# Optimization experiments

Measured on AMD Instinct MI355X. Metric: run time of the kernel, lower is better.

Reference implementation:

```python
import jax, jax.numpy as jnp
import numpy as np

# FP4 (e2m1) value table: sign bit in code>>3, magnitude in code&7
FP4 = jnp.array([0.0, 0.5, 1.0, 1.5, 2.0, 3.0, 4.0, 6.0,
                 -0.0, -0.5, -1.0, -1.5, -2.0, -3.0, -4.0, -6.0], dtype=jnp.float32)
BLOCK = 32  # MX block size: one shared E8M0 scale per 32 elements


def _unpack(packed):
    # packed: int32 holding byte values 0..255; low nibble first
    lo = packed & 0xF
    hi = (packed >> 4) & 0xF
    return jnp.stack([lo, hi], axis=-1).reshape(*packed.shape[:-1], packed.shape[-1] * 2)


def _dequant(packed, sf):
    # packed: [..., N//2] packed FP4 codes; sf: [..., N//32] E8M0 exponents
    vals = FP4[_unpack(packed)]                       # [..., N]
    n = vals.shape[-1]
    scale = jnp.exp2(sf.astype(jnp.float32) - 127.0)  # [..., N//32]
    vals = vals.reshape(*vals.shape[:-1], n // BLOCK, BLOCK) * scale[..., None]
    return vals.reshape(*scale.shape[:-1], n)


def setup_inputs() -> dict:
    key = jax.random.key(0)
    ks = jax.random.split(key, 6)
    M, IN, OUT, R = 8192, 4096, 4096, 128
    return {
        "x_q": jax.random.randint(ks[0], (M, IN // 2), 0, 256, dtype=jnp.int32),
        "scales_x": jax.random.randint(ks[1], (M, IN // BLOCK), 120, 134, dtype=jnp.int32),
        "weight": jax.random.randint(ks[2], (OUT, IN // 2), 0, 256, dtype=jnp.int32),
        "SF_w": jax.random.randint(ks[3], (OUT * IN // BLOCK,), 120, 134, dtype=jnp.int32),
        "low_rank_weight": jax.random.randint(ks[4], (OUT, R // 2), 0, 256, dtype=jnp.int32),
        "SF_low_rank_weight": jax.random.randint(ks[5], (OUT * R // BLOCK,), 120, 134, dtype=jnp.int32),
    }


def reference(x_q, scales_x, weight, SF_w, low_rank_weight, SF_low_rank_weight):
    OUT = weight.shape[0]
    IN = weight.shape[1] * 2
    R = low_rank_weight.shape[1] * 2  # 128
    # Low-rank path: first R unpacked features of x (R//2 packed bytes, R//32 scale blocks)
    x_lr = _dequant(x_q[:, :R // 2], scales_x[:, :R // BLOCK])                    # [M, R]
    W_lr = _dequant(low_rank_weight, SF_low_rank_weight.reshape(OUT, R // BLOCK))  # [OUT, R]
    out = jnp.einsum('mr,or->mo', x_lr, W_lr, preferred_element_type=jnp.float32)
    # Main 4-bit matmul fused with the low-rank correction
    x = _dequant(x_q, scales_x)                               # [M, IN]
    W = _dequant(weight, SF_w.reshape(OUT, IN // BLOCK))      # [OUT, IN]
    out = out + jnp.einsum('mi,oi->mo', x, W, preferred_element_type=jnp.float32)
    return out
```

## Files before the change

### kernel.cpp

```cpp
#include <hip/hip_runtime.h>
#include <hip/hip_bf16.h>
#include <stdint.h>


#define M_DIM 8192
#define N_DIM 4096
#define K_MAIN 4096
#define K_TOT 4224
#define NCHUNK 132
#define NT 33

#define XP_OFF   ((size_t)0)
#define WP_OFF   (XP_OFF + (size_t)NCHUNK * M_DIM * 16)
#define SXH_OFF  (WP_OFF + (size_t)NCHUNK * N_DIM * 16)
#define SWH_OFF  (SXH_OFF + (size_t)NT * 2 * M_DIM * 2)
#define WS_NEED  (SWH_OFF + (size_t)NT * 2 * N_DIM * 2)

typedef __attribute__((ext_vector_type(4))) float f32x4;
typedef __attribute__((ext_vector_type(16))) float f32x16;
typedef __attribute__((ext_vector_type(8))) short short8;
typedef __attribute__((ext_vector_type(8))) _Float16 half8;
typedef __attribute__((ext_vector_type(4))) int i32x4;
typedef __attribute__((ext_vector_type(8))) int i32x8;

#define PXP_N (NCHUNK * M_DIM)
#define PWP_N (NCHUNK * N_DIM)
#define TSX_N (NT * 2 * M_DIM / 2)
#define TSW_N (NT * 2 * N_DIM / 2)
#define PACK_TOTAL (PXP_N + PWP_N + TSX_N + TSW_N)

__device__ inline unsigned pack4(i32x4 q) {
    return (q.x & 255) | ((q.y & 255) << 8) | ((q.z & 255) << 16) |
           ((unsigned)(q.w & 255) << 24);
}

__global__ __launch_bounds__(256)
void pack_kernel(const int* __restrict__ xq, const int* __restrict__ sx,
                 const int* __restrict__ w, const int* __restrict__ sfw,
                 const int* __restrict__ lrw, const int* __restrict__ sflr,
                 uint8_t* __restrict__ ws) {
    int t = blockIdx.x * 256 + threadIdx.x;
    if (t < PXP_N) {
        const int g = t >> 13;
        const int m = t & 8191;
        const int gs = (g < 128) ? g : (g - 128);
        const int* src = xq + (size_t)m * 2048 + gs * 16;
        i32x4 o;
        o.x = (int)pack4(*(const i32x4*)(src + 0));
        o.y = (int)pack4(*(const i32x4*)(src + 4));
        o.z = (int)pack4(*(const i32x4*)(src + 8));
        o.w = (int)pack4(*(const i32x4*)(src + 12));
        *(i32x4*)(ws + XP_OFF + ((size_t)g * M_DIM + m) * 16) = o;
    } else if (t < PXP_N + PWP_N) {
        const int i = t - PXP_N;
        const int g = i >> 12;
        const int n = i & 4095;
        const int* src = (g < 128) ? (w + (size_t)n * 2048 + g * 16)
                                   : (lrw + (size_t)n * 64 + (g - 128) * 16);
        i32x4 o;
        o.x = (int)pack4(*(const i32x4*)(src + 0));
        o.y = (int)pack4(*(const i32x4*)(src + 4));
        o.z = (int)pack4(*(const i32x4*)(src + 8));
        o.w = (int)pack4(*(const i32x4*)(src + 12));
        *(i32x4*)(ws + WP_OFF + ((size_t)g * N_DIM + n) * 16) = o;
    } else if (t < PXP_N + PWP_N + TSX_N) {
        int i = t - PXP_N - PWP_N;
        int plane = i >> 12;
        int kt = plane >> 1, h = plane & 1;
        int r2 = (i & 4095) << 1;
        int g0 = kt * 4 + h, g2 = g0 + 2;
        int s0 = (g0 < 128) ? g0 : g0 - 128;
        int s2 = (g2 < 128) ? g2 : g2 - 128;
        unsigned b0 = sx[(size_t)r2 * 128 + s0] & 255;
        unsigned b1 = sx[(size_t)r2 * 128 + s2] & 255;
        unsigned b2 = sx[(size_t)(r2 + 1) * 128 + s0] & 255;
        unsigned b3 = sx[(size_t)(r2 + 1) * 128 + s2] & 255;
        *(unsigned*)(ws + SXH_OFF + (size_t)i * 4) = b0 | (b1 << 8) | (b2 << 16) | (b3 << 24);
    } else if (t < PACK_TOTAL) {
        int i = t - PXP_N - PWP_N - TSX_N;
        int plane = i >> 11;
        int kt = plane >> 1, h = plane & 1;
        int r2 = (i & 2047) << 1;
        int g0 = kt * 4 + h, g2 = g0 + 2;
        unsigned b0, b1, b2, b3;
        if (g0 < 128) { b0 = sfw[(size_t)r2 * 128 + g0] & 255; b2 = sfw[(size_t)(r2 + 1) * 128 + g0] & 255; }
        else          { b0 = sflr[(size_t)r2 * 4 + (g0 - 128)] & 255; b2 = sflr[(size_t)(r2 + 1) * 4 + (g0 - 128)] & 255; }
        if (g2 < 128) { b1 = sfw[(size_t)r2 * 128 + g2] & 255; b3 = sfw[(size_t)(r2 + 1) * 128 + g2] & 255; }
        else          { b1 = sflr[(size_t)r2 * 4 + (g2 - 128)] & 255; b3 = sflr[(size_t)(r2 + 1) * 4 + (g2 - 128)] & 255; }
        *(unsigned*)(ws + SWH_OFF + (size_t)i * 4) = b0 | (b1 << 8) | (b2 << 16) | (b3 << 24);
    }
}

__device__ inline void gload_lds16(const void* g, void* l) {
    __builtin_amdgcn_global_load_lds(
        (const __attribute__((address_space(1))) unsigned int*)g,
        (__attribute__((address_space(3))) unsigned int*)l, 16, 0, 0);
}

__device__ inline void stage_tile(const uint8_t* __restrict__ xp,
                                  const uint8_t* __restrict__ wp,
                                  int bm, int bn, int tt,
                                  uint8_t (*As)[256][16], uint8_t (*Bs)[256][16],
                                  int wid, int lane) {
    const int c = wid & 3;
    if (wid < 4) {
        const uint8_t* g = xp + ((size_t)(tt * 4 + c) * M_DIM + bm + lane) * 16;
#pragma unroll
        for (int q = 0; q < 4; ++q)
            gload_lds16(g + (size_t)q * 64 * 16, &As[c][q * 64][0]);
    } else {
        const uint8_t* g = wp + ((size_t)(tt * 4 + c) * N_DIM + bn + lane) * 16;
#pragma unroll
        for (int q = 0; q < 4; ++q)
            gload_lds16(g + (size_t)q * 64 * 16, &Bs[c][q * 64][0]);
    }
}

__device__ inline void load_scales(const uint8_t* __restrict__ sxH,
                                   const uint8_t* __restrict__ swH,
                                   int bm, int bn, int tt, int* sa, int* sb,
                                   int wr, int wc, int lane) {
    const int h = lane >> 5, r = lane & 31;
    const uint8_t* px = sxH + (size_t)((tt * 2 + h) * M_DIM + bm + wr * 128 + r) * 2;
#pragma unroll
    for (int mi = 0; mi < 4; ++mi) sa[mi] = *(const unsigned short*)(px + mi * 64);
    const uint8_t* pw = swH + (size_t)((tt * 2 + h) * N_DIM + bn + wc * 64 + r) * 2;
#pragma unroll
    for (int ni = 0; ni < 2; ++ni) sb[ni] = *(const unsigned short*)(pw + ni * 64);
}

template <int KK>
__device__ inline void compute_phase(const uint8_t (*As)[256][16],
                                     const uint8_t (*Bs)[256][16],
                                     f32x16 (&acc)[4][2], const int* sa, const int* sb,
                                     int wr, int wc, int lane) {
    const int h = lane >> 5, r = lane & 31;
    const int c = KK * 2 + h;
    i32x4 af[4], bf[2];
#pragma unroll
    for (int mi = 0; mi < 4; ++mi)
        af[mi] = *(const i32x4*)&As[c][wr * 128 + mi * 32 + r][0];
#pragma unroll
    for (int ni = 0; ni < 2; ++ni)
        bf[ni] = *(const i32x4*)&Bs[c][wc * 64 + ni * 32 + r][0];
    __builtin_amdgcn_s_setprio(1);
#pragma unroll
    for (int mi = 0; mi < 4; ++mi)
#pragma unroll
        for (int ni = 0; ni < 2; ++ni) {
            i32x8 a8 = {af[mi].x, af[mi].y, af[mi].z, af[mi].w, 0, 0, 0, 0};
            i32x8 b8 = {bf[ni].x, bf[ni].y, bf[ni].z, bf[ni].w, 0, 0, 0, 0};
            acc[mi][ni] = __builtin_amdgcn_mfma_scale_f32_32x32x64_f8f6f4(
                a8, b8, acc[mi][ni], 4, 4, KK, sa[mi], KK, sb[ni]);
        }
    __builtin_amdgcn_s_setprio(0);
}

__global__ __launch_bounds__(512, 2)
void l4b_mx3(const uint8_t* __restrict__ xp, const uint8_t* __restrict__ wp,
             const uint8_t* __restrict__ sxH, const uint8_t* __restrict__ swH,
             float* __restrict__ out) {
    __shared__ __align__(16) uint8_t As[2][4][256][16];
    __shared__ __align__(16) uint8_t Bs[2][4][256][16];

    const int tid = threadIdx.x;
    const int lane = tid & 63;
    const int wid = tid >> 6;
    const int wr = wid >> 2;
    const int wc = wid & 3;

    const int bid = blockIdx.x;
    const int wgid = (bid & 7) * 64 + (bid >> 3);
    const int bm = (wgid & 31) * 256;
    const int bn = (wgid >> 5) * 256;

    f32x16 acc[4][2] = {};
    int sa[4], sb[2], san[4], sbn[2];

    stage_tile(xp, wp, bm, bn, 0, As[0], Bs[0], wid, lane);
    load_scales(sxH, swH, bm, bn, 0, sa, sb, wr, wc, lane);
    __syncthreads();

    int cur = 0;
    for (int t = 0; t < NT - 1; ++t) {
        const int nxt = cur ^ 1;
        stage_tile(xp, wp, bm, bn, t + 1, As[nxt], Bs[nxt], wid, lane);
        load_scales(sxH, swH, bm, bn, t + 1, san, sbn, wr, wc, lane);
        compute_phase<0>(As[cur], Bs[cur], acc, sa, sb, wr, wc, lane);
        compute_phase<1>(As[cur], Bs[cur], acc, sa, sb, wr, wc, lane);
        __syncthreads();
        cur = nxt;
#pragma unroll
        for (int i = 0; i < 4; ++i) sa[i] = san[i];
        sb[0] = sbn[0]; sb[1] = sbn[1];
    }
    compute_phase<0>(As[cur], Bs[cur], acc, sa, sb, wr, wc, lane);
    compute_phase<1>(As[cur], Bs[cur], acc, sa, sb, wr, wc, lane);

#pragma unroll
    for (int mi = 0; mi < 4; ++mi)
#pragma unroll
        for (int ni = 0; ni < 2; ++ni) {
            const int col = bn + wc * 64 + ni * 32 + (lane & 31);
            const int rb = bm + wr * 128 + mi * 32 + 4 * (lane >> 5);
#pragma unroll
            for (int reg = 0; reg < 16; ++reg) {
                const int row = rb + (reg & 3) + 8 * (reg >> 2);
                out[(size_t)row * N_DIM + col] = acc[mi][ni][reg];
            }
        }
}

__device__ inline short8 dequant8_f16(i32x4 q, int sf) {
    unsigned b = (unsigned)q.x | ((unsigned)q.y << 8) |
                 ((unsigned)q.z << 16) | ((unsigned)q.w << 24);
    unsigned me = b & 0x07070707u;
    unsigned mo = (b >> 4) & 0x07070707u;
    const unsigned TLO = 0x3E3C3800u;
    const unsigned THI = 0x46444240u;
    unsigned He = __builtin_amdgcn_perm(THI, TLO, me);
    unsigned Ho = __builtin_amdgcn_perm(THI, TLO, mo);
    He |= (b & 0x08080808u) << 4;
    Ho |= (b & 0x80808080u);
    unsigned d0 = __builtin_amdgcn_perm(He, 0u, 0x05010400u);
    unsigned d1 = __builtin_amdgcn_perm(He, 0u, 0x07000600u);
    unsigned d2 = __builtin_amdgcn_perm(Ho, 0u, 0x05010400u);
    unsigned d3 = __builtin_amdgcn_perm(Ho, 0u, 0x07000600u);
    i32x4 di; di.x = (int)d0; di.y = (int)d1; di.z = (int)d2; di.w = (int)d3;
    half8 hh = __builtin_bit_cast(half8, di);
    unsigned short se = (unsigned short)((sf - 112) << 10);
    int srep = (int)((unsigned)se | ((unsigned)se << 16));
    i32x4 si; si.x = srep; si.y = srep; si.z = srep; si.w = srep;
    hh = hh * __builtin_bit_cast(half8, si);
    return __builtin_bit_cast(short8, hh);
}

__global__ __launch_bounds__(256)
void l4b_fused(const int* __restrict__ x_q, const int* __restrict__ scales_x,
               const int* __restrict__ weight, const int* __restrict__ SF_w,
               const int* __restrict__ lrw, const int* __restrict__ SF_lr,
               float* __restrict__ out) {
    __shared__ short As[128 * 64];
    __shared__ short Bs[128 * 64];
    const int tid = threadIdx.x;
    const int lane = tid & 63;
    const int wid = tid >> 6;
    const int wr = wid >> 1, wc = wid & 1;
    const int bm = blockIdx.y * 128, bn = blockIdx.x * 128;
    const int srow = tid >> 3;
    const int scol = (tid & 7) * 8;
    f32x4 acc[4][4] = {};
    for (int kt = 0; kt < K_TOT / 64; ++kt) {
        const int k0 = kt * 64;
        __syncthreads();
#pragma unroll
        for (int it = 0; it < 4; ++it) {
            const int row = it * 32 + srow;
            const int k = k0 + scol;
            const int ksrc = (k < K_MAIN) ? k : (k - K_MAIN);
            i32x4 q = *(const i32x4*)(x_q + (size_t)(bm + row) * 2048 + (ksrc >> 1));
            int sf = scales_x[(size_t)(bm + row) * 128 + (ksrc >> 5)];
            short8 v = dequant8_f16(q, sf);
            unsigned a = (unsigned)(row * 128 + scol * 2) ^ (unsigned)((row & 7) << 4);
            *(short8*)((char*)As + a) = v;
        }
#pragma unroll
        for (int it = 0; it < 4; ++it) {
            const int row = it * 32 + srow;
            const int k = k0 + scol;
            i32x4 q; int sf;
            if (k < K_MAIN) {
                q = *(const i32x4*)(weight + (size_t)(bn + row) * 2048 + (k >> 1));
                sf = SF_w[(size_t)(bn + row) * 128 + (k >> 5)];
            } else {
                q = *(const i32x4*)(lrw + (size_t)(bn + row) * 64 + ((k - K_MAIN) >> 1));
                sf = SF_lr[(size_t)(bn + row) * 4 + ((k - K_MAIN) >> 5)];
            }
            short8 v = dequant8_f16(q, sf);
            unsigned a = (unsigned)(row * 128 + scol * 2) ^ (unsigned)((row & 7) << 4);
            *(short8*)((char*)Bs + a) = v;
        }
        __syncthreads();
#pragma unroll
        for (int ks = 0; ks < 2; ++ks) {
            const int koff = ks * 32 + (lane >> 4) * 8;
            short8 af[4], bfr[4];
#pragma unroll
            for (int mi = 0; mi < 4; ++mi) {
                const int row = wr * 64 + mi * 16 + (lane & 15);
                unsigned a = (unsigned)(row * 128 + koff * 2) ^ (unsigned)((row & 7) << 4);
                af[mi] = *(const short8*)((const char*)As + a);
            }
#pragma unroll
            for (int ni = 0; ni < 4; ++ni) {
                const int row = wc * 64 + ni * 16 + (lane & 15);
                unsigned a = (unsigned)(row * 128 + koff * 2) ^ (unsigned)((row & 7) << 4);
                bfr[ni] = *(const short8*)((const char*)Bs + a);
            }
#pragma unroll
            for (int mi = 0; mi < 4; ++mi)
#pragma unroll
                for (int ni = 0; ni < 4; ++ni)
                    acc[mi][ni] = __builtin_amdgcn_mfma_f32_16x16x32_f16(
                        __builtin_bit_cast(half8, af[mi]),
                        __builtin_bit_cast(half8, bfr[ni]),
                        acc[mi][ni], 0, 0, 0);
        }
    }
#pragma unroll
    for (int mi = 0; mi < 4; ++mi)
#pragma unroll
        for (int ni = 0; ni < 4; ++ni) {
            const int col = bn + wc * 64 + ni * 16 + (lane & 15);
            const int row0 = bm + wr * 64 + mi * 16 + (lane >> 4) * 4;
#pragma unroll
            for (int r2 = 0; r2 < 4; ++r2)
                out[(size_t)(row0 + r2) * N_DIM + col] = acc[mi][ni][r2];
        }
}

extern "C" void kernel_launch(void* const* d_in, const int* in_sizes, int n_in,
                              void* d_out, int out_size, void* d_ws, size_t ws_size,
                              hipStream_t stream) {
    const int* x_q  = (const int*)d_in[0];
    const int* sx   = (const int*)d_in[1];
    const int* w    = (const int*)d_in[2];
    const int* sfw  = (const int*)d_in[3];
    const int* lrw  = (const int*)d_in[4];
    const int* sflr = (const int*)d_in[5];
    float* out = (float*)d_out;

    if (ws_size >= WS_NEED) {
        uint8_t* ws = (uint8_t*)d_ws;
        pack_kernel<<<(PACK_TOTAL + 255) / 256, 256, 0, stream>>>(x_q, sx, w, sfw, lrw, sflr, ws);
        l4b_mx3<<<(M_DIM / 256) * (N_DIM / 256), 512, 0, stream>>>(
            ws + XP_OFF, ws + WP_OFF, ws + SXH_OFF, ws + SWH_OFF, out);
    } else {
        dim3 grid(N_DIM / 128, M_DIM / 128);
        l4b_fused<<<grid, dim3(256), 0, stream>>>(x_q, sx, w, sfw, lrw, sflr, out);
    }
}
```

Measured before the change: 119.1 us.

## Split MX-FP4 main loop into barrier-synchronized LDS/MFMA sub-phases

Restructures the double-buffered GEMM main loop into four sub-phases. Each sub-phase loads a smaller set of fragments from LDS and then issues four scaled FP4 MFMAs, with raw s_barrier and sched_barrier fences between them. This lets the waves in a workgroup alternate LDS reads and MFMA work in lockstep and cuts register pressure. It replaces __syncthreads with an explicit vmcnt wait plus a barrier, and changes the block-to-tile mapping so that bn varies fastest. In exchange it adds more barriers per iteration, which can stall waves if the phases are unbalanced.

```diff
diff --git a/kernel.cpp b/kernel.cpp
--- a/kernel.cpp
+++ b/kernel.cpp
@@ -22,6 +22,8 @@
 typedef __attribute__((ext_vector_type(8))) _Float16 half8;
 typedef __attribute__((ext_vector_type(4))) int i32x4;
 typedef __attribute__((ext_vector_type(8))) int i32x8;
+
+#define SBAR() asm volatile("s_barrier" ::: "memory")
 
 #define PXP_N (NCHUNK * M_DIM)
 #define PWP_N (NCHUNK * N_DIM)
@@ -130,34 +132,22 @@
 }
 
 template <int KK>
-__device__ inline void compute_phase(const uint8_t (*As)[256][16],
-                                     const uint8_t (*Bs)[256][16],
-                                     f32x16 (&acc)[4][2], const int* sa, const int* sb,
-                                     int wr, int wc, int lane) {
-    const int h = lane >> 5, r = lane & 31;
-    const int c = KK * 2 + h;
-    i32x4 af[4], bf[2];
-#pragma unroll
-    for (int mi = 0; mi < 4; ++mi)
-        af[mi] = *(const i32x4*)&As[c][wr * 128 + mi * 32 + r][0];
-#pragma unroll
-    for (int ni = 0; ni < 2; ++ni)
-        bf[ni] = *(const i32x4*)&Bs[c][wc * 64 + ni * 32 + r][0];
-    __builtin_amdgcn_s_setprio(1);
-#pragma unroll
-    for (int mi = 0; mi < 4; ++mi)
-#pragma unroll
-        for (int ni = 0; ni < 2; ++ni) {
-            i32x8 a8 = {af[mi].x, af[mi].y, af[mi].z, af[mi].w, 0, 0, 0, 0};
-            i32x8 b8 = {bf[ni].x, bf[ni].y, bf[ni].z, bf[ni].w, 0, 0, 0, 0};
-            acc[mi][ni] = __builtin_amdgcn_mfma_scale_f32_32x32x64_f8f6f4(
-                a8, b8, acc[mi][ni], 4, 4, KK, sa[mi], KK, sb[ni]);
-        }
-    __builtin_amdgcn_s_setprio(0);
+__device__ inline void mfma_quad(const i32x4* af, const i32x4* bf,
+                                 f32x16& accA0, f32x16& accA1,
+                                 f32x16& accB0, f32x16& accB1,
+                                 int s0, int s1, const int* sb) {
+    i32x8 a0 = {af[0].x, af[0].y, af[0].z, af[0].w, 0, 0, 0, 0};
+    i32x8 a1 = {af[1].x, af[1].y, af[1].z, af[1].w, 0, 0, 0, 0};
+    i32x8 b0 = {bf[0].x, bf[0].y, bf[0].z, bf[0].w, 0, 0, 0, 0};
+    i32x8 b1 = {bf[1].x, bf[1].y, bf[1].z, bf[1].w, 0, 0, 0, 0};
+    accA0 = __builtin_amdgcn_mfma_scale_f32_32x32x64_f8f6f4(a0, b0, accA0, 4, 4, KK, s0, KK, sb[0]);
+    accA1 = __builtin_amdgcn_mfma_scale_f32_32x32x64_f8f6f4(a0, b1, accA1, 4, 4, KK, s0, KK, sb[1]);
+    accB0 = __builtin_amdgcn_mfma_scale_f32_32x32x64_f8f6f4(a1, b0, accB0, 4, 4, KK, s1, KK, sb[0]);
+    accB1 = __builtin_amdgcn_mfma_scale_f32_32x32x64_f8f6f4(a1, b1, accB1, 4, 4, KK, s1, KK, sb[1]);
 }
 
 __global__ __launch_bounds__(512, 2)
-void l4b_mx3(const uint8_t* __restrict__ xp, const uint8_t* __restrict__ wp,
+void l4b_mx4(const uint8_t* __restrict__ xp, const uint8_t* __restrict__ wp,
              const uint8_t* __restrict__ sxH, const uint8_t* __restrict__ swH,
              float* __restrict__ out) {
     __shared__ __align__(16) uint8_t As[2][4][256][16];
@@ -171,31 +161,84 @@
 
     const int bid = blockIdx.x;
     const int wgid = (bid & 7) * 64 + (bid >> 3);
-    const int bm = (wgid & 31) * 256;
-    const int bn = (wgid >> 5) * 256;
+    const int bn = (wgid & 15) * 256;
+    const int bm = (wgid >> 4) * 256;
+
+    const int h = lane >> 5, r = lane & 31;
 
     f32x16 acc[4][2] = {};
     int sa[4], sb[2], san[4], sbn[2];
 
     stage_tile(xp, wp, bm, bn, 0, As[0], Bs[0], wid, lane);
     load_scales(sxH, swH, bm, bn, 0, sa, sb, wr, wc, lane);
-    __syncthreads();
+    asm volatile("s_waitcnt vmcnt(0)" ::: "memory");
+    SBAR();
 
     int cur = 0;
-    for (int t = 0; t < NT - 1; ++t) {
+    for (int t = 0; t < NT; ++t) {
         const int nxt = cur ^ 1;
-        stage_tile(xp, wp, bm, bn, t + 1, As[nxt], Bs[nxt], wid, lane);
-        load_scales(sxH, swH, bm, bn, t + 1, san, sbn, wr, wc, lane);
-        compute_phase<0>(As[cur], Bs[cur], acc, sa, sb, wr, wc, lane);
-        compute_phase<1>(As[cur], Bs[cur], acc, sa, sb, wr, wc, lane);
-        __syncthreads();
+        i32x4 bf0[2], bf1[2], af[2];
+
+        if (t + 1 < NT) {
+            stage_tile(xp, wp, bm, bn, t + 1, As[nxt], Bs[nxt], wid, lane);
+            load_scales(sxH, swH, bm, bn, t + 1, san, sbn, wr, wc, lane);
+        }
+#pragma unroll
+        for (int ni = 0; ni < 2; ++ni)
+            bf0[ni] = *(const i32x4*)&Bs[cur][h][wc * 64 + ni * 32 + r][0];
+#pragma unroll
+        for (int mi = 0; mi < 2; ++mi)
+            af[mi] = *(const i32x4*)&As[cur][h][wr * 128 + mi * 32 + r][0];
+        SBAR();
+        __builtin_amdgcn_sched_barrier(0);
+        __builtin_amdgcn_s_setprio(1);
+        mfma_quad<0>(af, bf0, acc[0][0], acc[0][1], acc[1][0], acc[1][1], sa[0], sa[1], sb);
+        __builtin_amdgcn_s_setprio(0);
+        __builtin_amdgcn_sched_barrier(0);
+        SBAR();
+
+#pragma unroll
+        for (int mi = 0; mi < 2; ++mi)
+            af[mi] = *(const i32x4*)&As[cur][h][wr * 128 + (mi + 2) * 32 + r][0];
+        SBAR();
+        __builtin_amdgcn_sched_barrier(0);
+        __builtin_amdgcn_s_setprio(1);
+        mfma_quad<0>(af, bf0, acc[2][0], acc[2][1], acc[3][0], acc[3][1], sa[2], sa[3], sb);
+        __builtin_amdgcn_s_setprio(0);
+        __builtin_amdgcn_sched_barrier(0);
+        SBAR();
+
+#pragma unroll
+        for (int ni = 0; ni < 2; ++ni)
+            bf1[ni] = *(const i32x4*)&Bs[cur][2 + h][wc * 64 + ni * 32 + r][0];
+#pragma unroll
+        for (int mi = 0; mi < 2; ++mi)
+            af[mi] = *(const i32x4*)&As[cur][2 + h][wr * 128 + mi * 32 + r][0];
+        SBAR();
+        __builtin_amdgcn_sched_barrier(0);
+        __builtin_amdgcn_s_setprio(1);
+        mfma_quad<1>(af, bf1, acc[0][0], acc[0][1], acc[1][0], acc[1][1], sa[0], sa[1], sb);
+        __builtin_amdgcn_s_setprio(0);
+        __builtin_amdgcn_sched_barrier(0);
+        SBAR();
+
+#pragma unroll
+        for (int mi = 0; mi < 2; ++mi)
+            af[mi] = *(const i32x4*)&As[cur][2 + h][wr * 128 + (mi + 2) * 32 + r][0];
+        SBAR();
+        __builtin_amdgcn_sched_barrier(0);
+        __builtin_amdgcn_s_setprio(1);
+        mfma_quad<1>(af, bf1, acc[2][0], acc[2][1], acc[3][0], acc[3][1], sa[2], sa[3], sb);
+        __builtin_amdgcn_s_setprio(0);
+        __builtin_amdgcn_sched_barrier(0);
+        asm volatile("s_waitcnt vmcnt(0)" ::: "memory");
+        SBAR();
+
         cur = nxt;
 #pragma unroll
         for (int i = 0; i < 4; ++i) sa[i] = san[i];
         sb[0] = sbn[0]; sb[1] = sbn[1];
     }
-    compute_phase<0>(As[cur], Bs[cur], acc, sa, sb, wr, wc, lane);
-    compute_phase<1>(As[cur], Bs[cur], acc, sa, sb, wr, wc, lane);
 
 #pragma unroll
     for (int mi = 0; mi < 4; ++mi)
@@ -333,7 +376,7 @@
     if (ws_size >= WS_NEED) {
         uint8_t* ws = (uint8_t*)d_ws;
         pack_kernel<<<(PACK_TOTAL + 255) / 256, 256, 0, stream>>>(x_q, sx, w, sfw, lrw, sflr, ws);
-        l4b_mx3<<<(M_DIM / 256) * (N_DIM / 256), 512, 0, stream>>>(
+        l4b_mx4<<<(M_DIM / 256) * (N_DIM / 256), 512, 0, stream>>>(
             ws + XP_OFF, ws + WP_OFF, ws + SXH_OFF, ws + SWH_OFF, out);
     } else {
         dim3 grid(N_DIM / 128, M_DIM / 128);
```

Result: no change. 120.5 us (+1.2%).

## Split tile staging into halves interleaved with MFMA phases using raw barriers

Applied to the files above, without the earlier changes.

Restructures the main loop of the MX-FP4 GEMM. Each K-tile's global-to-LDS prefetch is split into two halves, each issued next to one MFMA phase. Fragment LDS reads are hoisted ahead of the prefetch issue, and `__syncthreads` is replaced with raw s_barrier plus explicit vmcnt waits, with the epilogue phase folded into the loop. It also swaps the block rasterization so N varies fastest within a group, which changes L2 reuse of X versus W. The aim is better overlap of memory traffic with matrix math. The cost is more barriers per tile, which can stall waves if the overlap does not pay off.

```diff
diff --git a/kernel.cpp b/kernel.cpp
--- a/kernel.cpp
+++ b/kernel.cpp
@@ -22,6 +22,8 @@
 typedef __attribute__((ext_vector_type(8))) _Float16 half8;
 typedef __attribute__((ext_vector_type(4))) int i32x4;
 typedef __attribute__((ext_vector_type(8))) int i32x8;
+
+#define SBAR() asm volatile("s_barrier" ::: "memory")
 
 #define PXP_N (NCHUNK * M_DIM)
 #define PWP_N (NCHUNK * N_DIM)
@@ -97,22 +99,21 @@
         (__attribute__((address_space(3))) unsigned int*)l, 16, 0, 0);
 }
 
-__device__ inline void stage_tile(const uint8_t* __restrict__ xp,
+__device__ inline void stage_half(const uint8_t* __restrict__ xp,
                                   const uint8_t* __restrict__ wp,
-                                  int bm, int bn, int tt,
+                                  int bm, int bn, int tt, int half,
                                   uint8_t (*As)[256][16], uint8_t (*Bs)[256][16],
                                   int wid, int lane) {
     const int c = wid & 3;
+    const int q0 = half * 2;
     if (wid < 4) {
         const uint8_t* g = xp + ((size_t)(tt * 4 + c) * M_DIM + bm + lane) * 16;
-#pragma unroll
-        for (int q = 0; q < 4; ++q)
-            gload_lds16(g + (size_t)q * 64 * 16, &As[c][q * 64][0]);
+        gload_lds16(g + (size_t)q0 * 64 * 16, &As[c][q0 * 64][0]);
+        gload_lds16(g + (size_t)(q0 + 1) * 64 * 16, &As[c][(q0 + 1) * 64][0]);
     } else {
         const uint8_t* g = wp + ((size_t)(tt * 4 + c) * N_DIM + bn + lane) * 16;
-#pragma unroll
-        for (int q = 0; q < 4; ++q)
-            gload_lds16(g + (size_t)q * 64 * 16, &Bs[c][q * 64][0]);
+        gload_lds16(g + (size_t)q0 * 64 * 16, &Bs[c][q0 * 64][0]);
+        gload_lds16(g + (size_t)(q0 + 1) * 64 * 16, &Bs[c][(q0 + 1) * 64][0]);
     }
 }
 
@@ -130,34 +131,25 @@
 }
 
 template <int KK>
-__device__ inline void compute_phase(const uint8_t (*As)[256][16],
-                                     const uint8_t (*Bs)[256][16],
-                                     f32x16 (&acc)[4][2], const int* sa, const int* sb,
-                                     int wr, int wc, int lane) {
-    const int h = lane >> 5, r = lane & 31;
-    const int c = KK * 2 + h;
-    i32x4 af[4], bf[2];
+__device__ inline void mfma_oct(const i32x4* af, const i32x4* bf,
+                                f32x16 (&acc)[4][2], const int* sa, const int* sb) {
+    i32x8 a[4], b[2];
 #pragma unroll
     for (int mi = 0; mi < 4; ++mi)
-        af[mi] = *(const i32x4*)&As[c][wr * 128 + mi * 32 + r][0];
+        a[mi] = i32x8{af[mi].x, af[mi].y, af[mi].z, af[mi].w, 0, 0, 0, 0};
 #pragma unroll
     for (int ni = 0; ni < 2; ++ni)
-        bf[ni] = *(const i32x4*)&Bs[c][wc * 64 + ni * 32 + r][0];
-    __builtin_amdgcn_s_setprio(1);
+        b[ni] = i32x8{bf[ni].x, bf[ni].y, bf[ni].z, bf[ni].w, 0, 0, 0, 0};
 #pragma unroll
     for (int mi = 0; mi < 4; ++mi)
 #pragma unroll
-        for (int ni = 0; ni < 2; ++ni) {
-            i32x8 a8 = {af[mi].x, af[mi].y, af[mi].z, af[mi].w, 0, 0, 0, 0};
-            i32x8 b8 = {bf[ni].x, bf[ni].y, bf[ni].z, bf[ni].w, 0, 0, 0, 0};
+        for (int ni = 0; ni < 2; ++ni)
             acc[mi][ni] = __builtin_amdgcn_mfma_scale_f32_32x32x64_f8f6f4(
-                a8, b8, acc[mi][ni], 4, 4, KK, sa[mi], KK, sb[ni]);
-        }
-    __builtin_amdgcn_s_setprio(0);
+                a[mi], b[ni], acc[mi][ni], 4, 4, KK, sa[mi], KK, sb[ni]);
 }
 
 __global__ __launch_bounds__(512, 2)
-void l4b_mx3(const uint8_t* __restrict__ xp, const uint8_t* __restrict__ wp,
+void l4b_mx5(const uint8_t* __restrict__ xp, const uint8_t* __restrict__ wp,
              const uint8_t* __restrict__ sxH, const uint8_t* __restrict__ swH,
              float* __restrict__ out) {
     __shared__ __align__(16) uint8_t As[2][4][256][16];
@@ -171,31 +163,62 @@
 
     const int bid = blockIdx.x;
     const int wgid = (bid & 7) * 64 + (bid >> 3);
-    const int bm = (wgid & 31) * 256;
-    const int bn = (wgid >> 5) * 256;
+    const int bn = (wgid & 15) * 256;
+    const int bm = (wgid >> 4) * 256;
+
+    const int h = lane >> 5, r = lane & 31;
 
     f32x16 acc[4][2] = {};
     int sa[4], sb[2], san[4], sbn[2];
 
-    stage_tile(xp, wp, bm, bn, 0, As[0], Bs[0], wid, lane);
+    stage_half(xp, wp, bm, bn, 0, 0, As[0], Bs[0], wid, lane);
+    stage_half(xp, wp, bm, bn, 0, 1, As[0], Bs[0], wid, lane);
     load_scales(sxH, swH, bm, bn, 0, sa, sb, wr, wc, lane);
-    __syncthreads();
+    asm volatile("s_waitcnt vmcnt(0)" ::: "memory");
+    SBAR();
 
     int cur = 0;
-    for (int t = 0; t < NT - 1; ++t) {
+    for (int t = 0; t < NT; ++t) {
         const int nxt = cur ^ 1;
-        stage_tile(xp, wp, bm, bn, t + 1, As[nxt], Bs[nxt], wid, lane);
-        load_scales(sxH, swH, bm, bn, t + 1, san, sbn, wr, wc, lane);
-        compute_phase<0>(As[cur], Bs[cur], acc, sa, sb, wr, wc, lane);
-        compute_phase<1>(As[cur], Bs[cur], acc, sa, sb, wr, wc, lane);
-        __syncthreads();
+        const bool pre = (t + 1 < NT);
+        i32x4 af[4], bf[2];
+
+#pragma unroll
+        for (int mi = 0; mi < 4; ++mi)
+            af[mi] = *(const i32x4*)&As[cur][h][wr * 128 + mi * 32 + r][0];
+#pragma unroll
+        for (int ni = 0; ni < 2; ++ni)
+            bf[ni] = *(const i32x4*)&Bs[cur][h][wc * 64 + ni * 32 + r][0];
+        if (pre) {
+            stage_half(xp, wp, bm, bn, t + 1, 0, As[nxt], Bs[nxt], wid, lane);
+            load_scales(sxH, swH, bm, bn, t + 1, san, sbn, wr, wc, lane);
+        }
+        SBAR();
+        __builtin_amdgcn_s_setprio(1);
+        mfma_oct<0>(af, bf, acc, sa, sb);
+        __builtin_amdgcn_s_setprio(0);
+        SBAR();
+
+#pragma unroll
+        for (int mi = 0; mi < 4; ++mi)
+            af[mi] = *(const i32x4*)&As[cur][2 + h][wr * 128 + mi * 32 + r][0];
+#pragma unroll
+        for (int ni = 0; ni < 2; ++ni)
+            bf[ni] = *(const i32x4*)&Bs[cur][2 + h][wc * 64 + ni * 32 + r][0];
+        if (pre)
+            stage_half(xp, wp, bm, bn, t + 1, 1, As[nxt], Bs[nxt], wid, lane);
+        SBAR();
+        __builtin_amdgcn_s_setprio(1);
+        mfma_oct<1>(af, bf, acc, sa, sb);
+        __builtin_amdgcn_s_setprio(0);
+        asm volatile("s_waitcnt vmcnt(0)" ::: "memory");
+        SBAR();
+
         cur = nxt;
 #pragma unroll
         for (int i = 0; i < 4; ++i) sa[i] = san[i];
         sb[0] = sbn[0]; sb[1] = sbn[1];
     }
-    compute_phase<0>(As[cur], Bs[cur], acc, sa, sb, wr, wc, lane);
-    compute_phase<1>(As[cur], Bs[cur], acc, sa, sb, wr, wc, lane);
 
 #pragma unroll
     for (int mi = 0; mi < 4; ++mi)
@@ -333,7 +356,7 @@
     if (ws_size >= WS_NEED) {
         uint8_t* ws = (uint8_t*)d_ws;
         pack_kernel<<<(PACK_TOTAL + 255) / 256, 256, 0, stream>>>(x_q, sx, w, sfw, lrw, sflr, ws);
-        l4b_mx3<<<(M_DIM / 256) * (N_DIM / 256), 512, 0, stream>>>(
+        l4b_mx5<<<(M_DIM / 256) * (N_DIM / 256), 512, 0, stream>>>(
             ws + XP_OFF, ws + WP_OFF, ws + SXH_OFF, ws + SWH_OFF, out);
     } else {
         dim3 grid(N_DIM / 128, M_DIM / 128);
```

Measured after the change: 123.7 us. 1.04x slower.

## Restructure MX-FP4 GEMM main loop with raw barriers and pointer increments

Applied to the files above, without the earlier changes.

Rewrites the main loop of the scaled-MFMA GEMM. Global and scale pointers are now precomputed and advanced each iteration, and all LDS fragments for both K halves are loaded before the MFMAs are issued. __syncthreads is replaced by an explicit vmcnt wait plus s_barrier, and the peeled final iteration is folded into the loop. The block-to-tile mapping is also swapped so N varies fastest within a group. The aim is lower address arithmetic, better LDS/MFMA overlap and different L2 reuse, at the cost of more live registers and reliance on manual wait and barrier semantics.

```diff
diff --git a/kernel.cpp b/kernel.cpp
--- a/kernel.cpp
+++ b/kernel.cpp
@@ -22,6 +22,8 @@
 typedef __attribute__((ext_vector_type(8))) _Float16 half8;
 typedef __attribute__((ext_vector_type(4))) int i32x4;
 typedef __attribute__((ext_vector_type(8))) int i32x8;
+
+#define SBAR() asm volatile("s_barrier" ::: "memory")
 
 #define PXP_N (NCHUNK * M_DIM)
 #define PWP_N (NCHUNK * N_DIM)
@@ -97,67 +99,12 @@
         (__attribute__((address_space(3))) unsigned int*)l, 16, 0, 0);
 }
 
-__device__ inline void stage_tile(const uint8_t* __restrict__ xp,
-                                  const uint8_t* __restrict__ wp,
-                                  int bm, int bn, int tt,
-                                  uint8_t (*As)[256][16], uint8_t (*Bs)[256][16],
-                                  int wid, int lane) {
-    const int c = wid & 3;
-    if (wid < 4) {
-        const uint8_t* g = xp + ((size_t)(tt * 4 + c) * M_DIM + bm + lane) * 16;
-#pragma unroll
-        for (int q = 0; q < 4; ++q)
-            gload_lds16(g + (size_t)q * 64 * 16, &As[c][q * 64][0]);
-    } else {
-        const uint8_t* g = wp + ((size_t)(tt * 4 + c) * N_DIM + bn + lane) * 16;
-#pragma unroll
-        for (int q = 0; q < 4; ++q)
-            gload_lds16(g + (size_t)q * 64 * 16, &Bs[c][q * 64][0]);
-    }
-}
-
-__device__ inline void load_scales(const uint8_t* __restrict__ sxH,
-                                   const uint8_t* __restrict__ swH,
-                                   int bm, int bn, int tt, int* sa, int* sb,
-                                   int wr, int wc, int lane) {
-    const int h = lane >> 5, r = lane & 31;
-    const uint8_t* px = sxH + (size_t)((tt * 2 + h) * M_DIM + bm + wr * 128 + r) * 2;
-#pragma unroll
-    for (int mi = 0; mi < 4; ++mi) sa[mi] = *(const unsigned short*)(px + mi * 64);
-    const uint8_t* pw = swH + (size_t)((tt * 2 + h) * N_DIM + bn + wc * 64 + r) * 2;
-#pragma unroll
-    for (int ni = 0; ni < 2; ++ni) sb[ni] = *(const unsigned short*)(pw + ni * 64);
-}
-
-template <int KK>
-__device__ inline void compute_phase(const uint8_t (*As)[256][16],
-                                     const uint8_t (*Bs)[256][16],
-                                     f32x16 (&acc)[4][2], const int* sa, const int* sb,
-                                     int wr, int wc, int lane) {
-    const int h = lane >> 5, r = lane & 31;
-    const int c = KK * 2 + h;
-    i32x4 af[4], bf[2];
-#pragma unroll
-    for (int mi = 0; mi < 4; ++mi)
-        af[mi] = *(const i32x4*)&As[c][wr * 128 + mi * 32 + r][0];
-#pragma unroll
-    for (int ni = 0; ni < 2; ++ni)
-        bf[ni] = *(const i32x4*)&Bs[c][wc * 64 + ni * 32 + r][0];
-    __builtin_amdgcn_s_setprio(1);
-#pragma unroll
-    for (int mi = 0; mi < 4; ++mi)
-#pragma unroll
-        for (int ni = 0; ni < 2; ++ni) {
-            i32x8 a8 = {af[mi].x, af[mi].y, af[mi].z, af[mi].w, 0, 0, 0, 0};
-            i32x8 b8 = {bf[ni].x, bf[ni].y, bf[ni].z, bf[ni].w, 0, 0, 0, 0};
-            acc[mi][ni] = __builtin_amdgcn_mfma_scale_f32_32x32x64_f8f6f4(
-                a8, b8, acc[mi][ni], 4, 4, KK, sa[mi], KK, sb[ni]);
-        }
-    __builtin_amdgcn_s_setprio(0);
+__device__ inline i32x8 zext8(i32x4 v) {
+    return i32x8{v.x, v.y, v.z, v.w, 0, 0, 0, 0};
 }
 
 __global__ __launch_bounds__(512, 2)
-void l4b_mx3(const uint8_t* __restrict__ xp, const uint8_t* __restrict__ wp,
+void l4b_mx6(const uint8_t* __restrict__ xp, const uint8_t* __restrict__ wp,
              const uint8_t* __restrict__ sxH, const uint8_t* __restrict__ swH,
              float* __restrict__ out) {
     __shared__ __align__(16) uint8_t As[2][4][256][16];
@@ -171,31 +118,109 @@
 
     const int bid = blockIdx.x;
     const int wgid = (bid & 7) * 64 + (bid >> 3);
-    const int bm = (wgid & 31) * 256;
-    const int bn = (wgid >> 5) * 256;
+    const int bn = (wgid & 15) * 256;
+    const int bm = (wgid >> 4) * 256;
+
+    const int h = lane >> 5, r = lane & 31;
+
+    const int cst = wid & 3;
+    const uint8_t* ga = (wid < 4)
+        ? xp + ((size_t)cst * M_DIM + bm + lane) * 16
+        : wp + ((size_t)cst * N_DIM + bn + lane) * 16;
+    const size_t gstride = (wid < 4) ? (size_t)4 * M_DIM * 16 : (size_t)4 * N_DIM * 16;
+    const uint8_t* psx = sxH + (size_t)(h * M_DIM + bm + wr * 128 + r) * 2;
+    const uint8_t* psw = swH + (size_t)(h * N_DIM + bn + wc * 64 + r) * 2;
+    const int laneoffA = h * 4096 + (wr * 128 + r) * 16;
+    const int laneoffB = h * 4096 + (wc * 64 + r) * 16;
 
     f32x16 acc[4][2] = {};
     int sa[4], sb[2], san[4], sbn[2];
 
-    stage_tile(xp, wp, bm, bn, 0, As[0], Bs[0], wid, lane);
-    load_scales(sxH, swH, bm, bn, 0, sa, sb, wr, wc, lane);
-    __syncthreads();
+    {
+        uint8_t(*T)[256][16] = (wid < 4) ? As[0] : Bs[0];
+#pragma unroll
+        for (int q = 0; q < 4; ++q)
+            gload_lds16(ga + q * 1024, &T[cst][q * 64][0]);
+        ga += gstride;
+    }
+#pragma unroll
+    for (int mi = 0; mi < 4; ++mi) sa[mi] = *(const unsigned short*)(psx + mi * 64);
+#pragma unroll
+    for (int ni = 0; ni < 2; ++ni) sb[ni] = *(const unsigned short*)(psw + ni * 64);
+    psx += 2 * M_DIM * 2;
+    psw += 2 * N_DIM * 2;
+    asm volatile("s_waitcnt vmcnt(0)" ::: "memory");
+    SBAR();
 
     int cur = 0;
-    for (int t = 0; t < NT - 1; ++t) {
+    for (int t = 0; t < NT; ++t) {
         const int nxt = cur ^ 1;
-        stage_tile(xp, wp, bm, bn, t + 1, As[nxt], Bs[nxt], wid, lane);
-        load_scales(sxH, swH, bm, bn, t + 1, san, sbn, wr, wc, lane);
-        compute_phase<0>(As[cur], Bs[cur], acc, sa, sb, wr, wc, lane);
-        compute_phase<1>(As[cur], Bs[cur], acc, sa, sb, wr, wc, lane);
-        __syncthreads();
+
+        if (t + 1 < NT) {
+            uint8_t(*T)[256][16] = (wid < 4) ? As[nxt] : Bs[nxt];
+#pragma unroll
+            for (int q = 0; q < 4; ++q)
+                gload_lds16(ga + q * 1024, &T[cst][q * 64][0]);
+            ga += gstride;
+#pragma unroll
+            for (int mi = 0; mi < 4; ++mi) san[mi] = *(const unsigned short*)(psx + mi * 64);
+#pragma unroll
+            for (int ni = 0; ni < 2; ++ni) sbn[ni] = *(const unsigned short*)(psw + ni * 64);
+            psx += 2 * M_DIM * 2;
+            psw += 2 * N_DIM * 2;
+        }
+
+        const char* pa = (const char*)As + cur * 16384 + laneoffA;
+        const char* pb = (const char*)Bs + cur * 16384 + laneoffB;
+        i32x4 af0[4], af1[4], bf0[2], bf1[2];
+#pragma unroll
+        for (int mi = 0; mi < 4; ++mi) {
+            af0[mi] = *(const i32x4*)(pa + mi * 512);
+            af1[mi] = *(const i32x4*)(pa + 8192 + mi * 512);
+        }
+#pragma unroll
+        for (int ni = 0; ni < 2; ++ni) {
+            bf0[ni] = *(const i32x4*)(pb + ni * 512);
+            bf1[ni] = *(const i32x4*)(pb + 8192 + ni * 512);
+        }
+
+        __builtin_amdgcn_s_setprio(1);
+        {
+            i32x8 a8[4], b8[2];
+#pragma unroll
+            for (int mi = 0; mi < 4; ++mi) a8[mi] = zext8(af0[mi]);
+#pragma unroll
+            for (int ni = 0; ni < 2; ++ni) b8[ni] = zext8(bf0[ni]);
+#pragma unroll
+            for (int mi = 0; mi < 4; ++mi)
+#pragma unroll
+                for (int ni = 0; ni < 2; ++ni)
+                    acc[mi][ni] = __builtin_amdgcn_mfma_scale_f32_32x32x64_f8f6f4(
+                        a8[mi], b8[ni], acc[mi][ni], 4, 4, 0, sa[mi], 0, sb[ni]);
+        }
+        {
+            i32x8 a8[4], b8[2];
+#pragma unroll
+            for (int mi = 0; mi < 4; ++mi) a8[mi] = zext8(af1[mi]);
+#pragma unroll
+            for (int ni = 0; ni < 2; ++ni) b8[ni] = zext8(bf1[ni]);
+#pragma unroll
+            for (int mi = 0; mi < 4; ++mi)
+#pragma unroll
+                for (int ni = 0; ni < 2; ++ni)
+                    acc[mi][ni] = __builtin_amdgcn_mfma_scale_f32_32x32x64_f8f6f4(
+                        a8[mi], b8[ni], acc[mi][ni], 4, 4, 1, sa[mi], 1, sb[ni]);
+        }
+        __builtin_amdgcn_s_setprio(0);
+
+        asm volatile("s_waitcnt vmcnt(0)" ::: "memory");
+        SBAR();
+
         cur = nxt;
 #pragma unroll
         for (int i = 0; i < 4; ++i) sa[i] = san[i];
         sb[0] = sbn[0]; sb[1] = sbn[1];
     }
-    compute_phase<0>(As[cur], Bs[cur], acc, sa, sb, wr, wc, lane);
-    compute_phase<1>(As[cur], Bs[cur], acc, sa, sb, wr, wc, lane);
 
 #pragma unroll
     for (int mi = 0; mi < 4; ++mi)
@@ -333,7 +358,7 @@
     if (ws_size >= WS_NEED) {
         uint8_t* ws = (uint8_t*)d_ws;
         pack_kernel<<<(PACK_TOTAL + 255) / 256, 256, 0, stream>>>(x_q, sx, w, sfw, lrw, sflr, ws);
-        l4b_mx3<<<(M_DIM / 256) * (N_DIM / 256), 512, 0, stream>>>(
+        l4b_mx6<<<(M_DIM / 256) * (N_DIM / 256), 512, 0, stream>>>(
             ws + XP_OFF, ws + WP_OFF, ws + SXH_OFF, ws + SWH_OFF, out);
     } else {
         dim3 grid(N_DIM / 128, M_DIM / 128);
```

Result: no change. 120.3 us (+1.0%).
